# Kernel optimization log

Hardware: AMD Instinct MI355X
Metric: run time of the kernel (lower is better)

Reference implementation:

```python
import jax, jax.numpy as jnp
import numpy as np

B, S, D = 16, 2048, 256

def setup_inputs() -> dict:
    key = jax.random.key(0)
    ks = jax.random.split(key, 7)
    scale = 1.0 / np.sqrt(D)
    return {
        "x": jax.random.normal(ks[0], (B, S, D), dtype=jnp.float32),
        "Wq": jax.random.normal(ks[1], (D, D), dtype=jnp.float32) * scale,
        "bq": jax.random.normal(ks[2], (D,), dtype=jnp.float32) * 0.01,
        "Wk": jax.random.normal(ks[3], (D, D), dtype=jnp.float32) * scale,
        "bk": jax.random.normal(ks[4], (D,), dtype=jnp.float32) * 0.01,
        "Wv": jax.random.normal(ks[5], (D, D), dtype=jnp.float32) * scale,
        "bv": jax.random.normal(ks[6], (D,), dtype=jnp.float32) * 0.01,
    }

def reference(x, Wq, bq, Wk, bk, Wv, bv):
    # q,k,v: [B,S,D]
    q = x @ Wq + bq
    k = x @ Wk + bk
    v = x @ Wv + bv
    inv_sqrt_d = jnp.asarray(1.0 / np.sqrt(x.shape[-1]), dtype=x.dtype)
    energy = jnp.einsum('bqd,bkd->bqk', q, k) * inv_sqrt_d  # [B,S,S]
    attn = jax.nn.softmax(energy, axis=-1)
    weighted = jnp.einsum('bqk,bkd->bqd', attn, v)  # [B,S,D]
    return weighted.sum(axis=1)  # [B,D]
```

## Files before the change

kernel.cpp:

```cpp
#include <hip/hip_runtime.h>
#include <hip/hip_bf16.h>

typedef __bf16 bf16_t;
typedef bf16_t bf16x8 __attribute__((ext_vector_type(8)));
typedef bf16_t bf16x4 __attribute__((ext_vector_type(4)));
typedef float  f32x4  __attribute__((ext_vector_type(4)));

constexpr int S = 2048, D = 256;


__device__ __forceinline__ float fast_exp2(float x) {
    return __builtin_amdgcn_exp2f(x);
}

__global__ void wt_kernel(const float* __restrict__ Wq, const float* __restrict__ Wk,
                          const float* __restrict__ Wv, bf16_t* __restrict__ wtf) {
    int idx = blockIdx.x * 256 + threadIdx.x;
    int w    = idx >> 13;
    int rem  = idx & 8191;
    int nt   = rem >> 9;
    int rem2 = rem & 511;
    int ks   = rem2 >> 6;
    int lane = rem2 & 63;
    int lm = lane & 15, lg = lane >> 4;
    const float* Wsrc = (w == 0) ? Wq : (w == 1) ? Wk : Wv;
    int col = nt * 16 + lm, krow = ks * 32 + lg * 8;
    bf16x8 o;
#pragma unroll
    for (int j = 0; j < 8; j++) o[j] = (bf16_t)Wsrc[(krow + j) * 256 + col];
    *(bf16x8*)(wtf + (size_t)idx * 8) = o;
}

__global__ __launch_bounds__(256) void proj_kernel(
    const float* __restrict__ x, const bf16_t* __restrict__ wtf,
    const float* __restrict__ bq, const float* __restrict__ bk, const float* __restrict__ bv,
    bf16_t* __restrict__ qo, bf16_t* __restrict__ ko, bf16_t* __restrict__ vo) {
    __shared__ float xs[2][128 * 36];
    int w    = blockIdx.y;
    int tid  = threadIdx.x;
    int wave = tid >> 6, lane = tid & 63, lm = lane & 15, lg = lane >> 4;
    int m0   = blockIdx.x * 128;
    const bf16_t* wb   = wtf + w * 65536;
    const float*  bias = (w == 0) ? bq : (w == 1) ? bk : bv;

    f32x4 acc[2][16];
#pragma unroll
    for (int s = 0; s < 2; s++)
#pragma unroll
        for (int nt = 0; nt < 16; nt++) acc[s][nt] = f32x4{0.f, 0.f, 0.f, 0.f};

    float4 stg[4];
#pragma unroll
    for (int u = 0; u < 4; u++) {
        int f = u * 256 + tid, row = f >> 3, c4 = f & 7;
        stg[u] = *(const float4*)(x + (size_t)(m0 + row) * 256 + c4 * 4);
    }

    for (int ks = 0; ks < 8; ks++) {
        int p = ks & 1;
#pragma unroll
        for (int u = 0; u < 4; u++) {
            int f = u * 256 + tid, row = f >> 3, c4 = f & 7;
            *(float4*)&xs[p][row * 36 + c4 * 4] = stg[u];
        }
        if (ks < 7) {
#pragma unroll
            for (int u = 0; u < 4; u++) {
                int f = u * 256 + tid, row = f >> 3, c4 = f & 7;
                stg[u] = *(const float4*)(x + (size_t)(m0 + row) * 256 + (ks + 1) * 32 + c4 * 4);
            }
        }
        __syncthreads();
        bf16x8 af[2];
#pragma unroll
        for (int s = 0; s < 2; s++) {
            const float* sp = &xs[p][(wave * 32 + s * 16 + lm) * 36 + lg * 8];
            float4 h0 = *(const float4*)sp;
            float4 h1 = *(const float4*)(sp + 4);
            af[s][0] = (bf16_t)h0.x; af[s][1] = (bf16_t)h0.y;
            af[s][2] = (bf16_t)h0.z; af[s][3] = (bf16_t)h0.w;
            af[s][4] = (bf16_t)h1.x; af[s][5] = (bf16_t)h1.y;
            af[s][6] = (bf16_t)h1.z; af[s][7] = (bf16_t)h1.w;
        }
#pragma unroll
        for (int nt = 0; nt < 16; nt++) {
            bf16x8 bfr = *(const bf16x8*)(wb + (size_t)(nt * 8 + ks) * 512 + lane * 8);
            acc[0][nt] = __builtin_amdgcn_mfma_f32_16x16x32_bf16(af[0], bfr, acc[0][nt], 0, 0, 0);
            acc[1][nt] = __builtin_amdgcn_mfma_f32_16x16x32_bf16(af[1], bfr, acc[1][nt], 0, 0, 0);
        }
    }

    int bglob = m0 >> 11;
    int qb0   = ((m0 & 2047) >> 4) + wave * 2;
#pragma unroll
    for (int s = 0; s < 2; s++) {
#pragma unroll
        for (int nt = 0; nt < 16; nt++) {
            int col = nt * 16 + lm;
            float bval = bias[col];
            if (w == 2) {
#pragma unroll
                for (int r = 0; r < 4; r++) {
                    int m = m0 + wave * 32 + s * 16 + lg * 4 + r;
                    int ss = m & 2047;
                    vo[((size_t)(bglob * 2048 + ss)) * 256 + col] = (bf16_t)(acc[s][nt][r] + bval);
                }
            } else {
                bf16_t* dst = (w == 0) ? qo : ko;
                int ks_t = col >> 5, lg_t = (col >> 3) & 3, j_t = col & 7;
#pragma unroll
                for (int r = 0; r < 4; r++) {
                    dst[((size_t)((bglob * 128 + qb0 + s) * 8 + ks_t)) * 512
                        + (lg_t * 16 + lg * 4 + r) * 8 + j_t] = (bf16_t)(acc[s][nt][r] + bval);
                }
            }
        }
    }
}

template <int PASS>
__global__ __launch_bounds__(256) void attn_pass(
    const bf16_t* __restrict__ q, const bf16_t* __restrict__ kmat,
    float* __restrict__ lpart, float* __restrict__ wpart) {
    __shared__ bf16_t kst[2][8192];
    __shared__ float  wacc[4][1024];

    int tid  = threadIdx.x;
    int wave = tid >> 6, lane = tid & 63, lm = lane & 15, lg = lane >> 4;
    int i  = blockIdx.x;
    int b  = ((i & 7) << 1) | ((i >> 8) & 1);
    int qt = (i >> 4) & 15;
    int kh = (i >> 3) & 1;

    bf16x8 af[2][8];
#pragma unroll
    for (int s = 0; s < 2; s++) {
        const bf16_t* qb = q + ((size_t)((b * 128 + qt * 8 + wave * 2 + s) * 8)) * 512;
#pragma unroll
        for (int ks = 0; ks < 8; ks++)
            af[s][ks] = *(const bf16x8*)(qb + ks * 512 + lane * 8);
    }

    float rinv[2][4];
    if (PASS == 2) {
#pragma unroll
        for (int s = 0; s < 2; s++)
#pragma unroll
            for (int r = 0; r < 4; r++) {
                int row = qt * 128 + wave * 32 + s * 16 + lg * 4 + r;
                float l = lpart[(size_t)b * 2048 + row] + lpart[(size_t)(16 + b) * 2048 + row];
                rinv[s][r] = 1.0f / l;
            }
    }

    float lsum[2][4];
#pragma unroll
    for (int s = 0; s < 2; s++)
#pragma unroll
        for (int r = 0; r < 4; r++) lsum[s][r] = 0.f;

    constexpr float SCL = 0.0625f * 1.44269504f;
    const bf16_t* kb_base = kmat + (size_t)(b * 128 + kh * 64) * 4096;

    bf16x8 stg[4];
#pragma unroll
    for (int u = 0; u < 4; u++)
        stg[u] = *(const bf16x8*)(kb_base + (size_t)(u * 256 + tid) * 8);

    for (int t = 0; t < 32; t++) {
        int p = t & 1;
#pragma unroll
        for (int u = 0; u < 4; u++)
            *(bf16x8*)&kst[p][(u * 256 + tid) * 8] = stg[u];
        if (t < 31) {
#pragma unroll
            for (int u = 0; u < 4; u++)
                stg[u] = *(const bf16x8*)(kb_base + (size_t)(t + 1) * 8192 + (u * 256 + tid) * 8);
        }
        __syncthreads();

        f32x4 sacc[2][2];
#pragma unroll
        for (int s = 0; s < 2; s++)
#pragma unroll
            for (int kb = 0; kb < 2; kb++) sacc[s][kb] = f32x4{0.f, 0.f, 0.f, 0.f};
#pragma unroll
        for (int ks = 0; ks < 8; ks++) {
#pragma unroll
            for (int kb = 0; kb < 2; kb++) {
                bf16x8 bfr = *(const bf16x8*)&kst[p][(kb * 8 + ks) * 512 + lane * 8];
                sacc[0][kb] = __builtin_amdgcn_mfma_f32_16x16x32_bf16(af[0][ks], bfr, sacc[0][kb], 0, 0, 0);
                sacc[1][kb] = __builtin_amdgcn_mfma_f32_16x16x32_bf16(af[1][ks], bfr, sacc[1][kb], 0, 0, 0);
            }
        }

        if (PASS == 1) {
#pragma unroll
            for (int s = 0; s < 2; s++)
#pragma unroll
                for (int kb = 0; kb < 2; kb++)
#pragma unroll
                    for (int r = 0; r < 4; r++)
                        lsum[s][r] += fast_exp2(sacc[s][kb][r] * SCL);
        } else {
            float wv[2] = {0.f, 0.f};
#pragma unroll
            for (int s = 0; s < 2; s++)
#pragma unroll
                for (int kb = 0; kb < 2; kb++)
#pragma unroll
                    for (int r = 0; r < 4; r++)
                        wv[kb] += fast_exp2(sacc[s][kb][r] * SCL) * rinv[s][r];
#pragma unroll
            for (int kb = 0; kb < 2; kb++) {
                float vsum = wv[kb];
                vsum += __shfl_xor(vsum, 16);
                vsum += __shfl_xor(vsum, 32);
                if (lg == 0) wacc[wave][t * 32 + kb * 16 + lm] = vsum;
            }
        }
    }

    if (PASS == 1) {
#pragma unroll
        for (int s = 0; s < 2; s++)
#pragma unroll
            for (int r = 0; r < 4; r++) {
                float v = lsum[s][r];
                v += __shfl_xor(v, 1);
                v += __shfl_xor(v, 2);
                v += __shfl_xor(v, 4);
                v += __shfl_xor(v, 8);
                if (lm == 0) {
                    int row = qt * 128 + wave * 32 + s * 16 + lg * 4 + r;
                    lpart[(size_t)(kh * 16 + b) * 2048 + row] = v;
                }
            }
    } else {
        __syncthreads();
        f32x4 sum = *(const f32x4*)&wacc[0][tid * 4];
#pragma unroll
        for (int w2 = 1; w2 < 4; w2++) {
            f32x4 t2 = *(const f32x4*)&wacc[w2][tid * 4];
#pragma unroll
            for (int u = 0; u < 4; u++) sum[u] += t2[u];
        }
        *(f32x4*)&wpart[(size_t)(qt * 16 + b) * 2048 + kh * 1024 + tid * 4] = sum;
    }
}

__global__ __launch_bounds__(1024) void gemv_kernel(
    const float* __restrict__ wpart, const bf16_t* __restrict__ v, float* __restrict__ out) {
    __shared__ float ldsw[2048];
    __shared__ float psum[16][256];
    int b = blockIdx.x, tid = threadIdx.x;
#pragma unroll
    for (int u = 0; u < 2; u++) {
        int kk = u * 1024 + tid;
        float s = 0.f;
#pragma unroll
        for (int qt = 0; qt < 16; qt++) s += wpart[(size_t)(qt * 16 + b) * 2048 + kk];
        ldsw[kk] = s;
    }
    __syncthreads();
    int wave = tid >> 6, lane = tid & 63;
    const bf16_t* vb = v + (size_t)b * 2048 * 256;
    f32x4 acc = f32x4{0.f, 0.f, 0.f, 0.f};
    for (int t = 0; t < 128; t++) {
        int kk = wave * 128 + t;
        float wv = ldsw[kk];
        bf16x4 vv = *(const bf16x4*)(vb + (size_t)kk * 256 + lane * 4);
#pragma unroll
        for (int u = 0; u < 4; u++) acc[u] += wv * (float)vv[u];
    }
    *(f32x4*)&psum[wave][lane * 4] = acc;
    __syncthreads();
    if (tid < 256) {
        float s = 0.f;
#pragma unroll
        for (int w2 = 0; w2 < 16; w2++) s += psum[w2][tid];
        out[b * 256 + tid] = s;
    }
}

extern "C" void kernel_launch(void* const* d_in, const int* in_sizes, int n_in,
                              void* d_out, int out_size, void* d_ws, size_t ws_size,
                              hipStream_t stream) {
    const float* x  = (const float*)d_in[0];
    const float* Wq = (const float*)d_in[1];
    const float* bq = (const float*)d_in[2];
    const float* Wk = (const float*)d_in[3];
    const float* bk = (const float*)d_in[4];
    const float* Wv = (const float*)d_in[5];
    const float* bv = (const float*)d_in[6];
    float* out = (float*)d_out;

    char* ws = (char*)d_ws;
    bf16_t* wtf   = (bf16_t*)(ws);
    bf16_t* q     = (bf16_t*)(ws + 393216);
    bf16_t* kmat  = (bf16_t*)(ws + 17170432);
    bf16_t* v     = (bf16_t*)(ws + 33947648);
    float*  lpart = (float*) (ws + 50724864);
    float*  wpart = (float*) (ws + 50987008);

    wt_kernel<<<dim3(96), dim3(256), 0, stream>>>(Wq, Wk, Wv, wtf);
    proj_kernel<<<dim3(256, 3), dim3(256), 0, stream>>>(x, wtf, bq, bk, bv, q, kmat, v);
    attn_pass<1><<<dim3(512), dim3(256), 0, stream>>>(q, kmat, lpart, wpart);
    attn_pass<2><<<dim3(512), dim3(256), 0, stream>>>(q, kmat, lpart, wpart);
    gemv_kernel<<<dim3(16), dim3(1024), 0, stream>>>(wpart, v, out);
}
```

Baseline: 225.9 us.

## Stage projection stores via LDS, retile attention to 512 threads, split gemv

The projection epilogue now writes results into shared memory and then emits 16-byte vector stores, replacing scattered 2-byte global writes. Attention blocks grow to 8 waves covering 256 query rows and a quarter of the keys each, with partial softmax sums combined across four key splits. The single 16-block gemv is replaced by a 128-block gemv plus a small reduction kernel to spread the final weighted-V product over more CUs. The extra kernel launch and the added LDS traffic and barrier in the projection are the costs paid for this.

New measurement: 221.7 us. About the same (-1.8%).

```diff
diff --git a/kernel.cpp b/kernel.cpp
--- a/kernel.cpp
+++ b/kernel.cpp
@@ -3,7 +3,6 @@
 
 typedef __bf16 bf16_t;
 typedef bf16_t bf16x8 __attribute__((ext_vector_type(8)));
-typedef bf16_t bf16x4 __attribute__((ext_vector_type(4)));
 typedef float  f32x4  __attribute__((ext_vector_type(4)));
 
 constexpr int S = 2048, D = 256;
@@ -90,52 +89,56 @@
         }
     }
 
+    __syncthreads();
+    bf16_t* sb = ((bf16_t*)&xs[0][0]) + wave * 4480;
     int bglob = m0 >> 11;
-    int qb0   = ((m0 & 2047) >> 4) + wave * 2;
 #pragma unroll
     for (int s = 0; s < 2; s++) {
 #pragma unroll
         for (int nt = 0; nt < 16; nt++) {
             int col = nt * 16 + lm;
             float bval = bias[col];
-            if (w == 2) {
-#pragma unroll
-                for (int r = 0; r < 4; r++) {
-                    int m = m0 + wave * 32 + s * 16 + lg * 4 + r;
-                    int ss = m & 2047;
-                    vo[((size_t)(bglob * 2048 + ss)) * 256 + col] = (bf16_t)(acc[s][nt][r] + bval);
-                }
-            } else {
-                bf16_t* dst = (w == 0) ? qo : ko;
-                int ks_t = col >> 5, lg_t = (col >> 3) & 3, j_t = col & 7;
-#pragma unroll
-                for (int r = 0; r < 4; r++) {
-                    dst[((size_t)((bglob * 128 + qb0 + s) * 8 + ks_t)) * 512
-                        + (lg_t * 16 + lg * 4 + r) * 8 + j_t] = (bf16_t)(acc[s][nt][r] + bval);
-                }
+#pragma unroll
+            for (int r = 0; r < 4; r++)
+                sb[(lg * 4 + r) * 280 + col] = (bf16_t)(acc[s][nt][r] + bval);
+        }
+        if (w == 2) {
+            int ssrow = (m0 & 2047) + wave * 32 + s * 16 + lm;
+#pragma unroll
+            for (int ks = 0; ks < 8; ks++) {
+                bf16x8 v8 = *(const bf16x8*)&sb[lm * 280 + ks * 32 + lg * 8];
+                *(bf16x8*)(vo + ((size_t)(bglob * 2048 + ssrow)) * 256 + ks * 32 + lg * 8) = v8;
+            }
+        } else {
+            bf16_t* dst = (w == 0) ? qo : ko;
+            int qb = ((m0 & 2047) >> 4) + wave * 2 + s;
+#pragma unroll
+            for (int ks = 0; ks < 8; ks++) {
+                bf16x8 v8 = *(const bf16x8*)&sb[lm * 280 + ks * 32 + lg * 8];
+                *(bf16x8*)(dst + ((size_t)((bglob * 128 + qb) * 8 + ks)) * 512 + lane * 8) = v8;
             }
         }
     }
 }
 
 template <int PASS>
-__global__ __launch_bounds__(256) void attn_pass(
+__global__ __launch_bounds__(512) void attn_pass(
     const bf16_t* __restrict__ q, const bf16_t* __restrict__ kmat,
     float* __restrict__ lpart, float* __restrict__ wpart) {
     __shared__ bf16_t kst[2][8192];
-    __shared__ float  wacc[4][1024];
+    __shared__ float  wacc[8][512];
 
     int tid  = threadIdx.x;
     int wave = tid >> 6, lane = tid & 63, lm = lane & 15, lg = lane >> 4;
     int i  = blockIdx.x;
     int b  = ((i & 7) << 1) | ((i >> 8) & 1);
-    int qt = (i >> 4) & 15;
-    int kh = (i >> 3) & 1;
+    int qt = (i >> 3) & 7;
+    int kh = (i >> 6) & 3;
 
     bf16x8 af[2][8];
 #pragma unroll
     for (int s = 0; s < 2; s++) {
-        const bf16_t* qb = q + ((size_t)((b * 128 + qt * 8 + wave * 2 + s) * 8)) * 512;
+        const bf16_t* qb = q + ((size_t)((b * 128 + qt * 16 + wave * 2 + s) * 8)) * 512;
 #pragma unroll
         for (int ks = 0; ks < 8; ks++)
             af[s][ks] = *(const bf16x8*)(qb + ks * 512 + lane * 8);
@@ -147,8 +150,11 @@
         for (int s = 0; s < 2; s++)
 #pragma unroll
             for (int r = 0; r < 4; r++) {
-                int row = qt * 128 + wave * 32 + s * 16 + lg * 4 + r;
-                float l = lpart[(size_t)b * 2048 + row] + lpart[(size_t)(16 + b) * 2048 + row];
+                int row = qt * 256 + wave * 32 + s * 16 + lg * 4 + r;
+                float l = 0.f;
+#pragma unroll
+                for (int k2 = 0; k2 < 4; k2++)
+                    l += lpart[(size_t)(k2 * 16 + b) * 2048 + row];
                 rinv[s][r] = 1.0f / l;
             }
     }
@@ -160,22 +166,22 @@
         for (int r = 0; r < 4; r++) lsum[s][r] = 0.f;
 
     constexpr float SCL = 0.0625f * 1.44269504f;
-    const bf16_t* kb_base = kmat + (size_t)(b * 128 + kh * 64) * 4096;
-
-    bf16x8 stg[4];
-#pragma unroll
-    for (int u = 0; u < 4; u++)
-        stg[u] = *(const bf16x8*)(kb_base + (size_t)(u * 256 + tid) * 8);
-
-    for (int t = 0; t < 32; t++) {
+    const bf16_t* kb_base = kmat + (size_t)(b * 128 + kh * 32) * 4096;
+
+    bf16x8 stg[2];
+#pragma unroll
+    for (int u = 0; u < 2; u++)
+        stg[u] = *(const bf16x8*)(kb_base + (size_t)(u * 512 + tid) * 8);
+
+    for (int t = 0; t < 16; t++) {
         int p = t & 1;
 #pragma unroll
-        for (int u = 0; u < 4; u++)
-            *(bf16x8*)&kst[p][(u * 256 + tid) * 8] = stg[u];
-        if (t < 31) {
-#pragma unroll
-            for (int u = 0; u < 4; u++)
-                stg[u] = *(const bf16x8*)(kb_base + (size_t)(t + 1) * 8192 + (u * 256 + tid) * 8);
+        for (int u = 0; u < 2; u++)
+            *(bf16x8*)&kst[p][(u * 512 + tid) * 8] = stg[u];
+        if (t < 15) {
+#pragma unroll
+            for (int u = 0; u < 2; u++)
+                stg[u] = *(const bf16x8*)(kb_base + (size_t)(t + 1) * 8192 + (u * 512 + tid) * 8);
         }
         __syncthreads();
 
@@ -226,61 +232,49 @@
         for (int s = 0; s < 2; s++)
 #pragma unroll
             for (int r = 0; r < 4; r++) {
-                float v = lsum[s][r];
-                v += __shfl_xor(v, 1);
-                v += __shfl_xor(v, 2);
-                v += __shfl_xor(v, 4);
-                v += __shfl_xor(v, 8);
+                float v2 = lsum[s][r];
+                v2 += __shfl_xor(v2, 1);
+                v2 += __shfl_xor(v2, 2);
+                v2 += __shfl_xor(v2, 4);
+                v2 += __shfl_xor(v2, 8);
                 if (lm == 0) {
-                    int row = qt * 128 + wave * 32 + s * 16 + lg * 4 + r;
-                    lpart[(size_t)(kh * 16 + b) * 2048 + row] = v;
+                    int row = qt * 256 + wave * 32 + s * 16 + lg * 4 + r;
+                    lpart[(size_t)(kh * 16 + b) * 2048 + row] = v2;
                 }
             }
     } else {
         __syncthreads();
-        f32x4 sum = *(const f32x4*)&wacc[0][tid * 4];
-#pragma unroll
-        for (int w2 = 1; w2 < 4; w2++) {
-            f32x4 t2 = *(const f32x4*)&wacc[w2][tid * 4];
-#pragma unroll
-            for (int u = 0; u < 4; u++) sum[u] += t2[u];
-        }
-        *(f32x4*)&wpart[(size_t)(qt * 16 + b) * 2048 + kh * 1024 + tid * 4] = sum;
-    }
-}
-
-__global__ __launch_bounds__(1024) void gemv_kernel(
-    const float* __restrict__ wpart, const bf16_t* __restrict__ v, float* __restrict__ out) {
-    __shared__ float ldsw[2048];
-    __shared__ float psum[16][256];
-    int b = blockIdx.x, tid = threadIdx.x;
-#pragma unroll
-    for (int u = 0; u < 2; u++) {
-        int kk = u * 1024 + tid;
-        float s = 0.f;
-#pragma unroll
-        for (int qt = 0; qt < 16; qt++) s += wpart[(size_t)(qt * 16 + b) * 2048 + kk];
-        ldsw[kk] = s;
-    }
+        float sum = 0.f;
+#pragma unroll
+        for (int w2 = 0; w2 < 8; w2++) sum += wacc[w2][tid];
+        wpart[(size_t)(qt * 16 + b) * 2048 + kh * 512 + tid] = sum;
+    }
+}
+
+__global__ __launch_bounds__(256) void gemv_kernel(
+    const float* __restrict__ wpart, const bf16_t* __restrict__ v,
+    float* __restrict__ gpart) {
+    __shared__ float ldsw[256];
+    int b = blockIdx.x >> 3, kseg = blockIdx.x & 7, tid = threadIdx.x;
+    int key = kseg * 256 + tid;
+    float s = 0.f;
+#pragma unroll
+    for (int qt = 0; qt < 8; qt++) s += wpart[(size_t)(qt * 16 + b) * 2048 + key];
+    ldsw[tid] = s;
     __syncthreads();
-    int wave = tid >> 6, lane = tid & 63;
-    const bf16_t* vb = v + (size_t)b * 2048 * 256;
-    f32x4 acc = f32x4{0.f, 0.f, 0.f, 0.f};
-    for (int t = 0; t < 128; t++) {
-        int kk = wave * 128 + t;
-        float wv = ldsw[kk];
-        bf16x4 vv = *(const bf16x4*)(vb + (size_t)kk * 256 + lane * 4);
-#pragma unroll
-        for (int u = 0; u < 4; u++) acc[u] += wv * (float)vv[u];
-    }
-    *(f32x4*)&psum[wave][lane * 4] = acc;
-    __syncthreads();
-    if (tid < 256) {
-        float s = 0.f;
-#pragma unroll
-        for (int w2 = 0; w2 < 16; w2++) s += psum[w2][tid];
-        out[b * 256 + tid] = s;
-    }
+    const bf16_t* vb = v + ((size_t)b * 2048 + kseg * 256) * 256;
+    float acc = 0.f;
+#pragma unroll 4
+    for (int t = 0; t < 256; t++) acc += ldsw[t] * (float)vb[(size_t)t * 256 + tid];
+    gpart[(size_t)(kseg * 16 + b) * 256 + tid] = acc;
+}
+
+__global__ void reduce_kernel(const float* __restrict__ gpart, float* __restrict__ out) {
+    int b = blockIdx.x, d = threadIdx.x;
+    float t = 0.f;
+#pragma unroll
+    for (int ks = 0; ks < 8; ks++) t += gpart[(size_t)(ks * 16 + b) * 256 + d];
+    out[b * 256 + d] = t;
 }
 
 extern "C" void kernel_launch(void* const* d_in, const int* in_sizes, int n_in,
@@ -301,11 +295,13 @@
     bf16_t* kmat  = (bf16_t*)(ws + 17170432);
     bf16_t* v     = (bf16_t*)(ws + 33947648);
     float*  lpart = (float*) (ws + 50724864);
-    float*  wpart = (float*) (ws + 50987008);
+    float*  wpart = (float*) (ws + 51249152);
+    float*  gpart = (float*) (ws + 52297728);
 
     wt_kernel<<<dim3(96), dim3(256), 0, stream>>>(Wq, Wk, Wv, wtf);
     proj_kernel<<<dim3(256, 3), dim3(256), 0, stream>>>(x, wtf, bq, bk, bv, q, kmat, v);
-    attn_pass<1><<<dim3(512), dim3(256), 0, stream>>>(q, kmat, lpart, wpart);
-    attn_pass<2><<<dim3(512), dim3(256), 0, stream>>>(q, kmat, lpart, wpart);
-    gemv_kernel<<<dim3(16), dim3(1024), 0, stream>>>(wpart, v, out);
-}
+    attn_pass<1><<<dim3(512), dim3(512), 0, stream>>>(q, kmat, lpart, wpart);
+    attn_pass<2><<<dim3(512), dim3(512), 0, stream>>>(q, kmat, lpart, wpart);
+    gemv_kernel<<<dim3(128), dim3(256), 0, stream>>>(wpart, v, gpart);
+    reduce_kernel<<<dim3(16), dim3(256), 0, stream>>>(gpart, out);
+}
```
